# Performance work log

Hardware: AMD Instinct MI355X
Metric: run time of the kernel (lower is better)

## Reference

```python
import jax, jax.numpy as jnp
import numpy as np

N_NODES = 100000
N_EDGES = 1250000
D_IN = 64
D_H = 64
D_OUT = 32


def setup_inputs() -> dict:
    key = jax.random.key(0)
    ks = jax.random.split(key, 8)
    x = jax.random.normal(ks[0], (N_NODES, D_IN), dtype=jnp.float32)
    edge_index = jax.random.randint(ks[1], (2, N_EDGES), 0, N_NODES, dtype=jnp.int64)
    s = 0.1
    W1_l = jax.random.normal(ks[2], (D_H, D_IN), dtype=jnp.float32) * s
    W1_r = jax.random.normal(ks[3], (D_H, D_IN), dtype=jnp.float32) * s
    b1 = jnp.zeros((D_H,), dtype=jnp.float32)
    W2_l = jax.random.normal(ks[4], (D_OUT, D_H), dtype=jnp.float32) * s
    W2_r = jax.random.normal(ks[5], (D_OUT, D_H), dtype=jnp.float32) * s
    b2 = jnp.zeros((D_OUT,), dtype=jnp.float32)
    return {"x": x, "edge_index": edge_index, "W1_l": W1_l, "W1_r": W1_r,
            "b1": b1, "W2_l": W2_l, "W2_r": W2_r, "b2": b2}


def _sage_conv(x, src, dst, W_l, W_r, b):
    # PyG SAGEConv (aggr='mean', root_weight=True):
    #   out = lin_l(mean_{j in N(i)} x_j) + lin_r(x_i)
    n = x.shape[0]
    msg = x[src]                                            # [E, d] gather
    ssum = jax.ops.segment_sum(msg, dst, num_segments=n)    # [N, d]
    deg = jax.ops.segment_sum(jnp.ones((src.shape[0], 1), x.dtype), dst,
                              num_segments=n)               # [N, 1]
    mean = ssum / jnp.maximum(deg, 1.0)
    return mean @ W_l.T + b + x @ W_r.T


def reference(x, edge_index, W1_l, W1_r, b1, W2_l, W2_r, b2):
    src = edge_index[0]
    dst = edge_index[1]
    h = jax.nn.relu(_sage_conv(x, src, dst, W1_l, W1_r, b1))
    out = _sage_conv(h, src, dst, W2_l, W2_r, b2)
    return out
```

## Files before the change

### kernel.cpp

```cpp
#include <hip/hip_runtime.h>

#define N_NODES 100000
#define N_EDGES 1250000
#define D_IN 64
#define D_H 64
#define D_OUT 32

#define BUCKETS 196
#define GRP 512
#define PREP_NB 512
#define PREP_CH 2442
#define SCAP 48
#define BSTRIDE (PREP_NB*SCAP)
#define CSRCAP 8192

typedef __attribute__((ext_vector_type(8))) short bf16x8;
typedef __attribute__((ext_vector_type(4))) float f32x4;

__device__ __forceinline__ unsigned short f2bf(float f) {
    unsigned u = __float_as_uint(f);
    u = (u + 0x7fffu + ((u >> 16) & 1u)) >> 16;
    return (unsigned short)u;
}
__device__ __forceinline__ float bfhi(unsigned v) { return __uint_as_float(v & 0xffff0000u); }
__device__ __forceinline__ float bflo(unsigned v) { return __uint_as_float(v << 16); }


__global__ __launch_bounds__(256) void k_prep(const float* __restrict__ x,
                                              unsigned short* __restrict__ xh,
                                              const int* __restrict__ src,
                                              const int* __restrict__ dst,
                                              int* __restrict__ ebuf,
                                              int* __restrict__ pcnt) {
    __shared__ int ofs[BUCKETS];
    int t = threadIdx.x, b = blockIdx.x;
    for (int i = t; i < BUCKETS; i += 256) ofs[i] = 0;
    __syncthreads();

    const int TOT = N_NODES * 64 / 4;
    for (int i = b * 256 + t; i < TOT; i += PREP_NB * 256) {
        float4 v = *(const float4*)(x + (size_t)i * 4);
        uint2 u;
        u.x = (unsigned)f2bf(v.x) | ((unsigned)f2bf(v.y) << 16);
        u.y = (unsigned)f2bf(v.z) | ((unsigned)f2bf(v.w) << 16);
        *(uint2*)(xh + (size_t)i * 4) = u;
    }

    int e0 = b * PREP_CH;
    int e1 = e0 + PREP_CH; if (e1 > N_EDGES) e1 = N_EDGES;
    for (int e = e0 + t; e < e1; e += 256) {
        int s = src[e], d = dst[e];
        if ((unsigned)d >= N_NODES) continue;
        int sv = ((unsigned)s < N_NODES) ? s : 0;
        int bk = d >> 9;
        int r = atomicAdd(&ofs[bk], 1);
        if (r < SCAP) ebuf[bk * BSTRIDE + b * SCAP + r] = ((d & 511) << 17) | sv;
    }
    __syncthreads();
    for (int i = t; i < BUCKETS; i += 256) {
        int v = ofs[i]; if (v > SCAP) v = SCAP;
        pcnt[b * BUCKETS + i] = v;
    }
}

__global__ __launch_bounds__(256) void k_phb(const int* __restrict__ ebuf,
                                             const int* __restrict__ pcnt,
                                             int* __restrict__ rstart,
                                             int* __restrict__ degா,
                                             int* __restrict__ csr_src) {
    __shared__ int sedge[CSRCAP];
    __shared__ int pc[PREP_NB];
    __shared__ int cnt[GRP];
    __shared__ int part[256];
    int b = blockIdx.x, t = threadIdx.x;

    int c0 = pcnt[(2 * t) * BUCKETS + b];
    int c1 = pcnt[(2 * t + 1) * BUCKETS + b];
    int s = c0 + c1;
    part[t] = s;
    __syncthreads();
    for (int off = 1; off < 256; off <<= 1) {
        int u = (t >= off) ? part[t - off] : 0;
        __syncthreads();
        part[t] += u;
        __syncthreads();
    }
    int run = part[t] - s;
    pc[2 * t] = run;
    pc[2 * t + 1] = run + c0;
    int n = part[255]; if (n > CSRCAP) n = CSRCAP;
    for (int i = t; i < GRP; i += 256) cnt[i] = 0;
    {
        const int* sp = ebuf + b * BSTRIDE + (2 * t) * SCAP;
        int base = pc[2 * t];
        for (int j = 0; j < c0; ++j) if (base + j < CSRCAP) sedge[base + j] = sp[j];
        sp += SCAP;
        base = pc[2 * t + 1];
        for (int j = 0; j < c1; ++j) if (base + j < CSRCAP) sedge[base + j] = sp[j];
    }
    __syncthreads();
    for (int i = t; i < n; i += 256) atomicAdd(&cnt[sedge[i] >> 17], 1);
    __syncthreads();
    int d0 = cnt[2 * t], d1 = cnt[2 * t + 1];
    int s2 = d0 + d1;
    part[t] = s2;
    __syncthreads();
    for (int off = 1; off < 256; off <<= 1) {
        int u = (t >= off) ? part[t - off] : 0;
        __syncthreads();
        part[t] += u;
        __syncthreads();
    }
    int g0 = b * CSRCAP + part[t] - s2;
    int node0 = b * GRP + 2 * t;
    if (node0 < N_NODES)     { rstart[node0]     = g0;      degா[node0]     = d0; }
    if (node0 + 1 < N_NODES) { rstart[node0 + 1] = g0 + d0; degா[node0 + 1] = d1; }
    __syncthreads();
    cnt[2 * t] = g0;
    cnt[2 * t + 1] = g0 + d0;
    __syncthreads();
    for (int i = t; i < n; i += 256) {
        int v = sedge[i];
        int pos = atomicAdd(&cnt[v >> 17], 1);
        csr_src[pos] = v & 0x1FFFF;
    }
}

__global__ __launch_bounds__(256) void k_fgemm(
    const unsigned short* __restrict__ xh,
    const int* __restrict__ rstart, const int* __restrict__ degா,
    const int* __restrict__ csr_src,
    const float* __restrict__ W1l, const float* __restrict__ W1r,
    const float* __restrict__ b1,
    const float* __restrict__ W2l, const float* __restrict__ W2r,
    unsigned short* __restrict__ hWlh, float* __restrict__ hr)
{
    __shared__ short sWB1[4 * 4 * 64 * 8];
    __shared__ short sWB2[2 * 4 * 64 * 8];
    __shared__ short mt[64 * 72];

    int tid = threadIdx.x;
    for (int e = tid; e < 1024; e += 256) {
        int kc = e >> 8, nt = (e >> 6) & 3, ln = e & 63;
        int cc = ln & 15, qd = ln >> 4;
        int n = nt * 16 + cc, k0 = kc * 32 + qd * 8;
        const float* sp = (k0 < 64) ? (W1l + n * 64 + k0) : (W1r + n * 64 + (k0 - 64));
        short* dp = sWB1 + e * 8;
        #pragma unroll
        for (int j = 0; j < 8; ++j) dp[j] = (short)f2bf(sp[j]);
    }
    for (int e = tid; e < 512; e += 256) {
        int kc = e >> 8, nt = (e >> 6) & 3, ln = e & 63;
        int cc = ln & 15, qd = ln >> 4;
        int n = nt * 16 + cc, k0 = kc * 32 + qd * 8;
        const float* sp = (n < 32) ? (W2l + n * 64 + k0) : (W2r + (n - 32) * 64 + k0);
        short* dp = sWB2 + e * 8;
        #pragma unroll
        for (int j = 0; j < 8; ++j) dp[j] = (short)f2bf(sp[j]);
    }
    __syncthreads();

    int lane = tid & 63, wv = tid >> 6;
    int base = blockIdx.x * 64;

    {
        int c32 = lane & 31;
        int hb = lane & 32;
        const unsigned* xp = (const unsigned*)xh;
        for (int k = 0; k < 8; ++k) {
            int lr = k * 8 + wv * 2 + (hb >> 5);
            int row = base + lr;
            if (row < N_NODES) {
                int start = rstart[row];
                int dg = degா[row];
                int end = start + dg;
                float x0 = 0.f, y0 = 0.f, x1 = 0.f, y1 = 0.f;
                float x2 = 0.f, y2 = 0.f, x3 = 0.f, y3 = 0.f;
                for (int eb = start; eb < end; eb += 32) {
                    int nv = end - eb; if (nv > 32) nv = 32;
                    int sid = (c32 < nv) ? csr_src[eb + c32] : 0;
                    int j = 0;
                    for (; j + 4 <= nv; j += 4) {
                        int s0 = __shfl(sid, hb + j + 0, 64);
                        int s1 = __shfl(sid, hb + j + 1, 64);
                        int s2 = __shfl(sid, hb + j + 2, 64);
                        int s3 = __shfl(sid, hb + j + 3, 64);
                        unsigned v0 = xp[s0 * 32 + c32];
                        unsigned v1 = xp[s1 * 32 + c32];
                        unsigned v2 = xp[s2 * 32 + c32];
                        unsigned v3 = xp[s3 * 32 + c32];
                        x0 += bflo(v0); y0 += bfhi(v0);
                        x1 += bflo(v1); y1 += bfhi(v1);
                        x2 += bflo(v2); y2 += bfhi(v2);
                        x3 += bflo(v3); y3 += bfhi(v3);
                    }
                    for (; j < nv; ++j) {
                        int s = __shfl(sid, hb + j, 64);
                        unsigned v = xp[s * 32 + c32];
                        x0 += bflo(v); y0 += bfhi(v);
                    }
                }
                float rdeg = 1.0f / fmaxf((float)dg, 1.0f);
                float fx = ((x0 + x1) + (x2 + x3)) * rdeg;
                float fy = ((y0 + y1) + (y2 + y3)) * rdeg;
                *(unsigned*)(mt + lr * 72 + 2 * c32) =
                    (unsigned)f2bf(fx) | ((unsigned)f2bf(fy) << 16);
            }
        }
    }
    __syncthreads();

    int c = lane & 15, quad = lane >> 4;
    float bias[4];
    #pragma unroll
    for (int nt = 0; nt < 4; ++nt) bias[nt] = b1[nt * 16 + c];

    const bf16x8* B1 = (const bf16x8*)sWB1;
    const bf16x8* B2 = (const bf16x8*)sWB2;
    short* ht = mt + wv * 16 * 72;
    int r0 = base + wv * 16;

    bf16x8 a0 = *(const bf16x8*)(ht + c * 72 + quad * 8);
    bf16x8 a1 = *(const bf16x8*)(ht + c * 72 + 32 + quad * 8);
    int ra = r0 + c; if (ra > N_NODES - 1) ra = N_NODES - 1;
    const bf16x8* xrow = (const bf16x8*)(xh + (size_t)ra * 64);
    bf16x8 a2 = xrow[quad];
    bf16x8 a3 = xrow[4 + quad];

    f32x4 acc[4];
    #pragma unroll
    for (int nt = 0; nt < 4; ++nt) acc[nt] = (f32x4){0.f, 0.f, 0.f, 0.f};
    #pragma unroll
    for (int nt = 0; nt < 4; ++nt)
        acc[nt] = __builtin_amdgcn_mfma_f32_16x16x32_bf16(a0, B1[(0 * 4 + nt) * 64 + lane], acc[nt], 0, 0, 0);
    #pragma unroll
    for (int nt = 0; nt < 4; ++nt)
        acc[nt] = __builtin_amdgcn_mfma_f32_16x16x32_bf16(a1, B1[(1 * 4 + nt) * 64 + lane], acc[nt], 0, 0, 0);
    #pragma unroll
    for (int nt = 0; nt < 4; ++nt)
        acc[nt] = __builtin_amdgcn_mfma_f32_16x16x32_bf16(a2, B1[(2 * 4 + nt) * 64 + lane], acc[nt], 0, 0, 0);
    #pragma unroll
    for (int nt = 0; nt < 4; ++nt)
        acc[nt] = __builtin_amdgcn_mfma_f32_16x16x32_bf16(a3, B1[(3 * 4 + nt) * 64 + lane], acc[nt], 0, 0, 0);

    #pragma unroll
    for (int nt = 0; nt < 4; ++nt) {
        #pragma unroll
        for (int reg = 0; reg < 4; ++reg) {
            float hv = fmaxf(acc[nt][reg] + bias[nt], 0.0f);
            ht[(quad * 4 + reg) * 72 + nt * 16 + c] = (short)f2bf(hv);
        }
    }
    bf16x8 h0 = *(const bf16x8*)(ht + c * 72 + 0  + quad * 8);
    bf16x8 h1 = *(const bf16x8*)(ht + c * 72 + 32 + quad * 8);

    f32x4 acc2[4];
    #pragma unroll
    for (int nt = 0; nt < 4; ++nt) acc2[nt] = (f32x4){0.f, 0.f, 0.f, 0.f};
    #pragma unroll
    for (int nt = 0; nt < 4; ++nt)
        acc2[nt] = __builtin_amdgcn_mfma_f32_16x16x32_bf16(h0, B2[(0 * 4 + nt) * 64 + lane], acc2[nt], 0, 0, 0);
    #pragma unroll
    for (int nt = 0; nt < 4; ++nt)
        acc2[nt] = __builtin_amdgcn_mfma_f32_16x16x32_bf16(h1, B2[(1 * 4 + nt) * 64 + lane], acc2[nt], 0, 0, 0);

    #pragma unroll
    for (int nt = 0; nt < 4; ++nt) {
        #pragma unroll
        for (int reg = 0; reg < 4; ++reg) {
            int row = r0 + quad * 4 + reg;
            if (row < N_NODES) {
                if (nt < 2) hWlh[(size_t)row * 32 + nt * 16 + c] = f2bf(acc2[nt][reg]);
                else        hr[(size_t)row * 32 + (nt - 2) * 16 + c] = acc2[nt][reg];
            }
        }
    }
}

__global__ __launch_bounds__(256) void k_l2(
    const unsigned short* __restrict__ hWlh, const float* __restrict__ hr,
    const int* __restrict__ rstart, const int* __restrict__ degா,
    const int* __restrict__ csr_src,
    const float* __restrict__ b2, float* __restrict__ out)
{
    int lane = threadIdx.x & 63;
    int wv = threadIdx.x >> 6;
    int c = lane & 15;
    int qb = lane & 48;
    const unsigned* hp = (const unsigned*)hWlh;
    float2 b2v = ((const float2*)b2)[c];

    int node0 = blockIdx.x * 16 + wv * 4 + (qb >> 4);
    for (int row = node0; row < N_NODES; row += gridDim.x * 16) {
        int start = rstart[row];
        int dg = degா[row];
        int end = start + dg;
        float x0 = 0.f, y0 = 0.f, x1 = 0.f, y1 = 0.f;
        float x2 = 0.f, y2 = 0.f, x3 = 0.f, y3 = 0.f;
        for (int eb = start; eb < end; eb += 16) {
            int nv = end - eb; if (nv > 16) nv = 16;
            int sid = (c < nv) ? csr_src[eb + c] : 0;
            int j = 0;
            for (; j + 4 <= nv; j += 4) {
                int s0 = __shfl(sid, qb + j + 0, 64);
                int s1 = __shfl(sid, qb + j + 1, 64);
                int s2 = __shfl(sid, qb + j + 2, 64);
                int s3 = __shfl(sid, qb + j + 3, 64);
                unsigned v0 = hp[s0 * 16 + c];
                unsigned v1 = hp[s1 * 16 + c];
                unsigned v2 = hp[s2 * 16 + c];
                unsigned v3 = hp[s3 * 16 + c];
                x0 += bflo(v0); y0 += bfhi(v0);
                x1 += bflo(v1); y1 += bfhi(v1);
                x2 += bflo(v2); y2 += bfhi(v2);
                x3 += bflo(v3); y3 += bfhi(v3);
            }
            for (; j < nv; ++j) {
                int s = __shfl(sid, qb + j, 64);
                unsigned v = hp[s * 16 + c];
                x0 += bflo(v); y0 += bfhi(v);
            }
        }
        float fx = (x0 + x1) + (x2 + x3);
        float fy = (y0 + y1) + (y2 + y3);
        float rdeg = 1.0f / fmaxf((float)dg, 1.0f);
        float2 hv = ((const float2*)hr)[(size_t)row * 16 + c];
        float2 o;
        o.x = fmaf(fx, rdeg, hv.x + b2v.x);
        o.y = fmaf(fy, rdeg, hv.y + b2v.y);
        ((float2*)out)[(size_t)row * 16 + c] = o;
    }
}

extern "C" void kernel_launch(void* const* d_in, const int* in_sizes, int n_in,
                              void* d_out, int out_size, void* d_ws, size_t ws_size,
                              hipStream_t stream) {
    const float* x   = (const float*)d_in[0];
    const int*   ei  = (const int*)d_in[1];
    const float* W1l = (const float*)d_in[2];
    const float* W1r = (const float*)d_in[3];
    const float* b1  = (const float*)d_in[4];
    const float* W2l = (const float*)d_in[5];
    const float* W2r = (const float*)d_in[6];
    const float* b2  = (const float*)d_in[7];
    float* out = (float*)d_out;

    const int* src = ei;
    const int* dst = ei + N_EDGES;

    char* w = (char*)d_ws;
    int* rstart  = (int*)w;   w += sizeof(int) * (N_NODES + 4);
    int* deg     = (int*)w;   w += sizeof(int) * (N_NODES + 4);
    int* pcnt    = (int*)w;   w += sizeof(int) * (PREP_NB * BUCKETS);
    int* csr_src = (int*)w;   w += sizeof(int) * (BUCKETS * CSRCAP);
    int* ebuf    = (int*)w;   w += sizeof(int) * (BUCKETS * BSTRIDE);
    unsigned short* xh   = (unsigned short*)w; w += sizeof(short) * (size_t)N_NODES * 64;
    unsigned short* hWlh = (unsigned short*)w; w += sizeof(short) * (size_t)N_NODES * 32;
    float*          hr   = (float*)w;

    k_prep<<<PREP_NB, 256, 0, stream>>>(x, xh, src, dst, ebuf, pcnt);
    k_phb<<<BUCKETS, 256, 0, stream>>>(ebuf, pcnt, rstart, deg, csr_src);
    k_fgemm<<<(N_NODES + 63) / 64, 256, 0, stream>>>(
        xh, rstart, deg, csr_src, W1l, W1r, b1, W2l, W2r, hWlh, hr);
    k_l2<<<4096, 256, 0, stream>>>(hWlh, hr, rstart, deg, csr_src, b2, out);
}
```

Before: 215.4 us.

## Split fused layer-1 gather+GEMM into separate gather and GEMM kernels

Unfuses the layer-1 neighbor-mean gather from the MFMA GEMM kernel. A new grid-stride gather kernel writes bf16 means to a global buffer, and a separate GEMM kernel reads them alongside x. The aim is to keep the gather at full occupancy without the large shared-memory weight staging and the block-wide barrier between gather and GEMM. The cost is one extra kernel launch and a write-then-read round trip of a 100k×64 bf16 buffer through global memory. The same commit renames a parameter that contained a non-ASCII identifier.

```diff
diff --git a/kernel.cpp b/kernel.cpp
--- a/kernel.cpp
+++ b/kernel.cpp
@@ -66,7 +66,7 @@
 __global__ __launch_bounds__(256) void k_phb(const int* __restrict__ ebuf,
                                              const int* __restrict__ pcnt,
                                              int* __restrict__ rstart,
-                                             int* __restrict__ degா,
+                                             int* __restrict__ deg_,
                                              int* __restrict__ csr_src) {
     __shared__ int sedge[CSRCAP];
     __shared__ int pc[PREP_NB];
@@ -113,8 +113,8 @@
     }
     int g0 = b * CSRCAP + part[t] - s2;
     int node0 = b * GRP + 2 * t;
-    if (node0 < N_NODES)     { rstart[node0]     = g0;      degா[node0]     = d0; }
-    if (node0 + 1 < N_NODES) { rstart[node0 + 1] = g0 + d0; degா[node0 + 1] = d1; }
+    if (node0 < N_NODES)     { rstart[node0]     = g0;      deg_[node0]     = d0; }
+    if (node0 + 1 < N_NODES) { rstart[node0 + 1] = g0 + d0; deg_[node0 + 1] = d1; }
     __syncthreads();
     cnt[2 * t] = g0;
     cnt[2 * t + 1] = g0 + d0;
@@ -126,10 +126,58 @@
     }
 }
 
-__global__ __launch_bounds__(256) void k_fgemm(
+__global__ __launch_bounds__(256) void k_gather1(
     const unsigned short* __restrict__ xh,
-    const int* __restrict__ rstart, const int* __restrict__ degா,
+    const int* __restrict__ rstart, const int* __restrict__ deg_,
     const int* __restrict__ csr_src,
+    unsigned int* __restrict__ meanh)
+{
+    int lane = threadIdx.x & 63;
+    int wv = threadIdx.x >> 6;
+    int c = lane & 31;
+    int hb = lane & 32;
+    const unsigned* xp = (const unsigned*)xh;
+
+    int node0 = blockIdx.x * 8 + wv * 2 + (hb >> 5);
+    for (int row = node0; row < N_NODES; row += gridDim.x * 8) {
+        int start = rstart[row];
+        int dg = deg_[row];
+        int end = start + dg;
+        float x0 = 0.f, y0 = 0.f, x1 = 0.f, y1 = 0.f;
+        float x2 = 0.f, y2 = 0.f, x3 = 0.f, y3 = 0.f;
+        for (int eb = start; eb < end; eb += 32) {
+            int nv = end - eb; if (nv > 32) nv = 32;
+            int sid = (c < nv) ? csr_src[eb + c] : 0;
+            int j = 0;
+            for (; j + 4 <= nv; j += 4) {
+                int s0 = __shfl(sid, hb + j + 0, 64);
+                int s1 = __shfl(sid, hb + j + 1, 64);
+                int s2 = __shfl(sid, hb + j + 2, 64);
+                int s3 = __shfl(sid, hb + j + 3, 64);
+                unsigned v0 = xp[s0 * 32 + c];
+                unsigned v1 = xp[s1 * 32 + c];
+                unsigned v2 = xp[s2 * 32 + c];
+                unsigned v3 = xp[s3 * 32 + c];
+                x0 += bflo(v0); y0 += bfhi(v0);
+                x1 += bflo(v1); y1 += bfhi(v1);
+                x2 += bflo(v2); y2 += bfhi(v2);
+                x3 += bflo(v3); y3 += bfhi(v3);
+            }
+            for (; j < nv; ++j) {
+                int s = __shfl(sid, hb + j, 64);
+                unsigned v = xp[s * 32 + c];
+                x0 += bflo(v); y0 += bfhi(v);
+            }
+        }
+        float rdeg = 1.0f / fmaxf((float)dg, 1.0f);
+        float fx = ((x0 + x1) + (x2 + x3)) * rdeg;
+        float fy = ((y0 + y1) + (y2 + y3)) * rdeg;
+        meanh[(size_t)row * 32 + c] = (unsigned)f2bf(fx) | ((unsigned)f2bf(fy) << 16);
+    }
+}
+
+__global__ __launch_bounds__(256) void k_gemm1(
+    const unsigned short* __restrict__ xh, const unsigned short* __restrict__ meanh,
     const float* __restrict__ W1l, const float* __restrict__ W1r,
     const float* __restrict__ b1,
     const float* __restrict__ W2l, const float* __restrict__ W2r,
@@ -137,7 +185,7 @@
 {
     __shared__ short sWB1[4 * 4 * 64 * 8];
     __shared__ short sWB2[2 * 4 * 64 * 8];
-    __shared__ short mt[64 * 72];
+    __shared__ short htile[4][16 * 72];
 
     int tid = threadIdx.x;
     for (int e = tid; e < 1024; e += 256) {
@@ -160,56 +208,7 @@
     }
     __syncthreads();
 
-    int lane = tid & 63, wv = tid >> 6;
-    int base = blockIdx.x * 64;
-
-    {
-        int c32 = lane & 31;
-        int hb = lane & 32;
-        const unsigned* xp = (const unsigned*)xh;
-        for (int k = 0; k < 8; ++k) {
-            int lr = k * 8 + wv * 2 + (hb >> 5);
-            int row = base + lr;
-            if (row < N_NODES) {
-                int start = rstart[row];
-                int dg = degா[row];
-                int end = start + dg;
-                float x0 = 0.f, y0 = 0.f, x1 = 0.f, y1 = 0.f;
-                float x2 = 0.f, y2 = 0.f, x3 = 0.f, y3 = 0.f;
-                for (int eb = start; eb < end; eb += 32) {
-                    int nv = end - eb; if (nv > 32) nv = 32;
-                    int sid = (c32 < nv) ? csr_src[eb + c32] : 0;
-                    int j = 0;
-                    for (; j + 4 <= nv; j += 4) {
-                        int s0 = __shfl(sid, hb + j + 0, 64);
-                        int s1 = __shfl(sid, hb + j + 1, 64);
-                        int s2 = __shfl(sid, hb + j + 2, 64);
-                        int s3 = __shfl(sid, hb + j + 3, 64);
-                        unsigned v0 = xp[s0 * 32 + c32];
-                        unsigned v1 = xp[s1 * 32 + c32];
-                        unsigned v2 = xp[s2 * 32 + c32];
-                        unsigned v3 = xp[s3 * 32 + c32];
-                        x0 += bflo(v0); y0 += bfhi(v0);
-                        x1 += bflo(v1); y1 += bfhi(v1);
-                        x2 += bflo(v2); y2 += bfhi(v2);
-                        x3 += bflo(v3); y3 += bfhi(v3);
-                    }
-                    for (; j < nv; ++j) {
-                        int s = __shfl(sid, hb + j, 64);
-                        unsigned v = xp[s * 32 + c32];
-                        x0 += bflo(v); y0 += bfhi(v);
-                    }
-                }
-                float rdeg = 1.0f / fmaxf((float)dg, 1.0f);
-                float fx = ((x0 + x1) + (x2 + x3)) * rdeg;
-                float fy = ((y0 + y1) + (y2 + y3)) * rdeg;
-                *(unsigned*)(mt + lr * 72 + 2 * c32) =
-                    (unsigned)f2bf(fx) | ((unsigned)f2bf(fy) << 16);
-            }
-        }
-    }
-    __syncthreads();
-
+    int lane = tid & 63, w = tid >> 6;
     int c = lane & 15, quad = lane >> 4;
     float bias[4];
     #pragma unroll
@@ -217,61 +216,63 @@
 
     const bf16x8* B1 = (const bf16x8*)sWB1;
     const bf16x8* B2 = (const bf16x8*)sWB2;
-    short* ht = mt + wv * 16 * 72;
-    int r0 = base + wv * 16;
-
-    bf16x8 a0 = *(const bf16x8*)(ht + c * 72 + quad * 8);
-    bf16x8 a1 = *(const bf16x8*)(ht + c * 72 + 32 + quad * 8);
-    int ra = r0 + c; if (ra > N_NODES - 1) ra = N_NODES - 1;
-    const bf16x8* xrow = (const bf16x8*)(xh + (size_t)ra * 64);
-    bf16x8 a2 = xrow[quad];
-    bf16x8 a3 = xrow[4 + quad];
-
-    f32x4 acc[4];
-    #pragma unroll
-    for (int nt = 0; nt < 4; ++nt) acc[nt] = (f32x4){0.f, 0.f, 0.f, 0.f};
-    #pragma unroll
-    for (int nt = 0; nt < 4; ++nt)
-        acc[nt] = __builtin_amdgcn_mfma_f32_16x16x32_bf16(a0, B1[(0 * 4 + nt) * 64 + lane], acc[nt], 0, 0, 0);
-    #pragma unroll
-    for (int nt = 0; nt < 4; ++nt)
-        acc[nt] = __builtin_amdgcn_mfma_f32_16x16x32_bf16(a1, B1[(1 * 4 + nt) * 64 + lane], acc[nt], 0, 0, 0);
-    #pragma unroll
-    for (int nt = 0; nt < 4; ++nt)
-        acc[nt] = __builtin_amdgcn_mfma_f32_16x16x32_bf16(a2, B1[(2 * 4 + nt) * 64 + lane], acc[nt], 0, 0, 0);
-    #pragma unroll
-    for (int nt = 0; nt < 4; ++nt)
-        acc[nt] = __builtin_amdgcn_mfma_f32_16x16x32_bf16(a3, B1[(3 * 4 + nt) * 64 + lane], acc[nt], 0, 0, 0);
-
-    #pragma unroll
-    for (int nt = 0; nt < 4; ++nt) {
-        #pragma unroll
-        for (int reg = 0; reg < 4; ++reg) {
-            float hv = fmaxf(acc[nt][reg] + bias[nt], 0.0f);
-            ht[(quad * 4 + reg) * 72 + nt * 16 + c] = (short)f2bf(hv);
+    short* ht = htile[w];
+
+    for (int r0 = blockIdx.x * 64 + w * 16; r0 < N_NODES; r0 += gridDim.x * 64) {
+        int ra = r0 + c; if (ra > N_NODES - 1) ra = N_NODES - 1;
+        const bf16x8* mrow = (const bf16x8*)((const unsigned short*)meanh + (size_t)ra * 64);
+        const bf16x8* xrow = (const bf16x8*)(xh + (size_t)ra * 64);
+        bf16x8 a0 = mrow[quad];
+        bf16x8 a1 = mrow[4 + quad];
+        bf16x8 a2 = xrow[quad];
+        bf16x8 a3 = xrow[4 + quad];
+
+        f32x4 acc[4];
+        #pragma unroll
+        for (int nt = 0; nt < 4; ++nt) acc[nt] = (f32x4){0.f, 0.f, 0.f, 0.f};
+        #pragma unroll
+        for (int nt = 0; nt < 4; ++nt)
+            acc[nt] = __builtin_amdgcn_mfma_f32_16x16x32_bf16(a0, B1[(0 * 4 + nt) * 64 + lane], acc[nt], 0, 0, 0);
+        #pragma unroll
+        for (int nt = 0; nt < 4; ++nt)
+            acc[nt] = __builtin_amdgcn_mfma_f32_16x16x32_bf16(a1, B1[(1 * 4 + nt) * 64 + lane], acc[nt], 0, 0, 0);
+        #pragma unroll
+        for (int nt = 0; nt < 4; ++nt)
+            acc[nt] = __builtin_amdgcn_mfma_f32_16x16x32_bf16(a2, B1[(2 * 4 + nt) * 64 + lane], acc[nt], 0, 0, 0);
+        #pragma unroll
+        for (int nt = 0; nt < 4; ++nt)
+            acc[nt] = __builtin_amdgcn_mfma_f32_16x16x32_bf16(a3, B1[(3 * 4 + nt) * 64 + lane], acc[nt], 0, 0, 0);
+
+        #pragma unroll
+        for (int nt = 0; nt < 4; ++nt) {
+            #pragma unroll
+            for (int reg = 0; reg < 4; ++reg) {
+                float hv = fmaxf(acc[nt][reg] + bias[nt], 0.0f);
+                ht[(quad * 4 + reg) * 72 + nt * 16 + c] = (short)f2bf(hv);
+            }
         }
-    }
-    bf16x8 h0 = *(const bf16x8*)(ht + c * 72 + 0  + quad * 8);
-    bf16x8 h1 = *(const bf16x8*)(ht + c * 72 + 32 + quad * 8);
-
-    f32x4 acc2[4];
-    #pragma unroll
-    for (int nt = 0; nt < 4; ++nt) acc2[nt] = (f32x4){0.f, 0.f, 0.f, 0.f};
-    #pragma unroll
-    for (int nt = 0; nt < 4; ++nt)
-        acc2[nt] = __builtin_amdgcn_mfma_f32_16x16x32_bf16(h0, B2[(0 * 4 + nt) * 64 + lane], acc2[nt], 0, 0, 0);
-    #pragma unroll
-    for (int nt = 0; nt < 4; ++nt)
-        acc2[nt] = __builtin_amdgcn_mfma_f32_16x16x32_bf16(h1, B2[(1 * 4 + nt) * 64 + lane], acc2[nt], 0, 0, 0);
-
-    #pragma unroll
-    for (int nt = 0; nt < 4; ++nt) {
-        #pragma unroll
-        for (int reg = 0; reg < 4; ++reg) {
-            int row = r0 + quad * 4 + reg;
-            if (row < N_NODES) {
-                if (nt < 2) hWlh[(size_t)row * 32 + nt * 16 + c] = f2bf(acc2[nt][reg]);
-                else        hr[(size_t)row * 32 + (nt - 2) * 16 + c] = acc2[nt][reg];
+        bf16x8 h0 = *(const bf16x8*)(ht + c * 72 + 0  + quad * 8);
+        bf16x8 h1 = *(const bf16x8*)(ht + c * 72 + 32 + quad * 8);
+
+        f32x4 acc2[4];
+        #pragma unroll
+        for (int nt = 0; nt < 4; ++nt) acc2[nt] = (f32x4){0.f, 0.f, 0.f, 0.f};
+        #pragma unroll
+        for (int nt = 0; nt < 4; ++nt)
+            acc2[nt] = __builtin_amdgcn_mfma_f32_16x16x32_bf16(h0, B2[(0 * 4 + nt) * 64 + lane], acc2[nt], 0, 0, 0);
+        #pragma unroll
+        for (int nt = 0; nt < 4; ++nt)
+            acc2[nt] = __builtin_amdgcn_mfma_f32_16x16x32_bf16(h1, B2[(1 * 4 + nt) * 64 + lane], acc2[nt], 0, 0, 0);
+
+        #pragma unroll
+        for (int nt = 0; nt < 4; ++nt) {
+            #pragma unroll
+            for (int reg = 0; reg < 4; ++reg) {
+                int row = r0 + quad * 4 + reg;
+                if (row < N_NODES) {
+                    if (nt < 2) hWlh[(size_t)row * 32 + nt * 16 + c] = f2bf(acc2[nt][reg]);
+                    else        hr[(size_t)row * 32 + (nt - 2) * 16 + c] = acc2[nt][reg];
+                }
             }
         }
     }
@@ -279,7 +280,7 @@
 
 __global__ __launch_bounds__(256) void k_l2(
     const unsigned short* __restrict__ hWlh, const float* __restrict__ hr,
-    const int* __restrict__ rstart, const int* __restrict__ degா,
+    const int* __restrict__ rstart, const int* __restrict__ deg_,
     const int* __restrict__ csr_src,
     const float* __restrict__ b2, float* __restrict__ out)
 {
@@ -293,7 +294,7 @@
     int node0 = blockIdx.x * 16 + wv * 4 + (qb >> 4);
     for (int row = node0; row < N_NODES; row += gridDim.x * 16) {
         int start = rstart[row];
-        int dg = degா[row];
+        int dg = deg_[row];
         int end = start + dg;
         float x0 = 0.f, y0 = 0.f, x1 = 0.f, y1 = 0.f;
         float x2 = 0.f, y2 = 0.f, x3 = 0.f, y3 = 0.f;
@@ -354,13 +355,15 @@
     int* pcnt    = (int*)w;   w += sizeof(int) * (PREP_NB * BUCKETS);
     int* csr_src = (int*)w;   w += sizeof(int) * (BUCKETS * CSRCAP);
     int* ebuf    = (int*)w;   w += sizeof(int) * (BUCKETS * BSTRIDE);
-    unsigned short* xh   = (unsigned short*)w; w += sizeof(short) * (size_t)N_NODES * 64;
-    unsigned short* hWlh = (unsigned short*)w; w += sizeof(short) * (size_t)N_NODES * 32;
-    float*          hr   = (float*)w;
+    unsigned short* xh    = (unsigned short*)w; w += sizeof(short) * (size_t)N_NODES * 64;
+    unsigned int*   meanh = (unsigned int*)w;   w += sizeof(int)   * (size_t)N_NODES * 32;
+    unsigned short* hWlh  = (unsigned short*)w; w += sizeof(short) * (size_t)N_NODES * 32;
+    float*          hr    = (float*)w;
 
     k_prep<<<PREP_NB, 256, 0, stream>>>(x, xh, src, dst, ebuf, pcnt);
     k_phb<<<BUCKETS, 256, 0, stream>>>(ebuf, pcnt, rstart, deg, csr_src);
-    k_fgemm<<<(N_NODES + 63) / 64, 256, 0, stream>>>(
-        xh, rstart, deg, csr_src, W1l, W1r, b1, W2l, W2r, hWlh, hr);
+    k_gather1<<<4096, 256, 0, stream>>>(xh, rstart, deg, csr_src, meanh);
+    k_gemm1<<<(N_NODES + 63) / 64, 256, 0, stream>>>(
+        xh, (const unsigned short*)meanh, W1l, W1r, b1, W2l, W2r, hWlh, hr);
     k_l2<<<4096, 256, 0, stream>>>(hWlh, hr, rstart, deg, csr_src, b2, out);
 }
```

New measurement: 204.5 us. 1.05x faster.
